# Performance work log

Hardware: AMD Instinct MI355X
Metric: run time of the kernel (lower is better)

The kernel has to match this reference:

```python
import jax, jax.numpy as jnp
import numpy as np

B, S, D_IN, D_MID, D_OUT, V = 32, 512, 768, 128, 4, 100000
N = B * S  # static upper bound on number of unique (vocab_id, batch_id) pairs


def setup_inputs() -> dict:
    key = jax.random.key(0)
    k1, k2, k3, k4 = jax.random.split(key, 4)
    vocab_ids = jax.random.randint(k1, (B, S), 0, V)
    embeddings = jax.random.normal(k2, (B, S, D_IN), jnp.float32)
    # nn.Linear default init (kaiming-uniform-ish); exact distribution is irrelevant for correctness
    lin_bound = 1.0 / np.sqrt(D_IN)
    W1 = jax.random.uniform(k3, (D_IN, D_MID), jnp.float32, -lin_bound, lin_bound)
    b1 = jnp.zeros((D_MID,), jnp.float32)
    # kaiming_uniform_(a=sqrt(5)) on (V, D_MID, D_OUT): fan_in = D_MID*D_OUT, bound = 1/sqrt(fan_in)
    enc_bound = 1.0 / np.sqrt(D_MID * D_OUT)
    encoder_weights = jax.random.uniform(k4, (V, D_MID, D_OUT), jnp.float32, -enc_bound, enc_bound)
    return {"vocab_ids": vocab_ids, "embeddings": embeddings, "W1": W1, "b1": b1,
            "encoder_weights": encoder_weights}


def reference(vocab_ids, embeddings, W1, b1, encoder_weights):
    # Composite key = vocab_id * B + batch_id -> same lexicographic (vocab, batch) order
    # as torch.unique(dim=0) on stacked (vocab_id, batch_id) pairs.
    batch_ids = jnp.arange(B, dtype=vocab_ids.dtype)[:, None]            # (B,1)
    keys = (vocab_ids * B + batch_ids).reshape(-1)                        # (N,)
    # Static-size unique for jit; padded slots (fill) receive zero-sum embeddings.
    uniq_keys, inv = jnp.unique(keys, size=N, fill_value=0, return_inverse=True)
    flat_emb = embeddings.reshape(N, D_IN)
    summed = jax.ops.segment_sum(flat_emb, inv.reshape(-1), num_segments=N)  # (N, D_IN)
    h = jnp.tanh(summed @ W1 + b1)                                        # (N, D_MID)
    uniq_vocab = uniq_keys // B
    uniq_batch = uniq_keys % B
    Wtok = encoder_weights[uniq_vocab]                                    # (N, D_MID, D_OUT) gather
    encoded = jax.nn.sigmoid(jnp.einsum('bi,bio->bo', h, Wtok))           # (N, D_OUT)
    ids = jnp.stack([uniq_vocab, uniq_batch], axis=1)                     # (N, 2)
    return ids, encoded
```

## Files before the change

kernel.cpp:

```cpp
#include <hip/hip_runtime.h>
#include <hip/hip_bf16.h>

#define NELEM 16384
#define DIN 768
#define DMID 128
#define DOUT 4

typedef __attribute__((ext_vector_type(8))) short short8;
typedef __attribute__((ext_vector_type(4))) float f32x4;

__device__ __forceinline__ unsigned f2bf(float f) {
    unsigned u = __float_as_uint(f);
    return (u + 0x7FFFu + ((u >> 16) & 1u)) >> 16;
}


#define FAST_WS 557120

__global__ __launch_bounds__(256) void prep_kernel(
    const int* __restrict__ vocab_ids, const float* __restrict__ W1,
    unsigned* __restrict__ P0, unsigned* __restrict__ hist0,
    unsigned* __restrict__ histZ, unsigned short* __restrict__ WtG) {
    const int t = threadIdx.x;
    const int bx = blockIdx.x;
    if (bx < 64) {
        __shared__ unsigned h[256];
        h[t] = 0;
        int e = bx * 256 + t;
        unsigned word = ((unsigned)vocab_ids[e] << 14) | (unsigned)e;
        P0[e] = word;
        __syncthreads();
        atomicAdd(&h[(word >> 9) & 255u], 1u);
        __syncthreads();
        hist0[t * 64 + bx] = h[t];
        histZ[bx * 512 + t] = 0;
        histZ[bx * 512 + 256 + t] = 0;
    } else {
        int idx = (bx - 64) * 256 + t;
        int c = idx / DIN;
        int k = idx - c * DIN;
        WtG[idx] = (unsigned short)f2bf(W1[k * DMID + c]);
    }
}

template <int SHIFT, int NSHIFT, bool HASNEXT>
__global__ __launch_bounds__(256) void scatter_kernel(
    const unsigned* __restrict__ src, unsigned* __restrict__ dst,
    const unsigned* __restrict__ histCur, unsigned* __restrict__ histNext) {
    __shared__ unsigned base_lds[256];
    __shared__ unsigned whist[4 * 256];
    __shared__ unsigned wsum[4];
    const int t = threadIdx.x;
    const int blk = blockIdx.x;
    const int lane = t & 63;
    const int w = t >> 6;

    unsigned x = src[blk * 256 + t];
    unsigned d = (x >> SHIFT) & 255u;

    whist[t] = 0; whist[256 + t] = 0; whist[512 + t] = 0; whist[768 + t] = 0;

    unsigned rowsum = 0, myprefix = 0;
    const uint4* row = (const uint4*)(histCur + t * 64);
#pragma unroll
    for (int q = 0; q < 16; ++q) {
        uint4 h4 = row[q];
        int b = q * 4;
        rowsum += h4.x + h4.y + h4.z + h4.w;
        if (b + 0 < blk) myprefix += h4.x;
        if (b + 1 < blk) myprefix += h4.y;
        if (b + 2 < blk) myprefix += h4.z;
        if (b + 3 < blk) myprefix += h4.w;
    }
    unsigned inc = rowsum;
#pragma unroll
    for (int off = 1; off < 64; off <<= 1) {
        unsigned y = __shfl_up(inc, off);
        if (lane >= off) inc += y;
    }
    if (lane == 63) wsum[w] = inc;
    __syncthreads();
    unsigned wo = 0;
    for (int w2 = 0; w2 < w; ++w2) wo += wsum[w2];
    base_lds[t] = wo + (inc - rowsum) + myprefix;

    unsigned long long m = ~0ull;
#pragma unroll
    for (int bit = 0; bit < 8; ++bit) {
        unsigned long long bb = __ballot((d >> bit) & 1u);
        m &= ((d >> bit) & 1u) ? bb : ~bb;
    }
    int inrank = __popcll(m & ((1ull << lane) - 1ull));
    if (inrank == 0) whist[w * 256 + d] = (unsigned)__popcll(m);
    __syncthreads();
    unsigned cross = 0;
    for (int w2 = 0; w2 < w; ++w2) cross += whist[w2 * 256 + d];
    unsigned dstpos = base_lds[d] + cross + (unsigned)inrank;
    dst[dstpos] = x;
    if (HASNEXT) {
        unsigned dn = (x >> NSHIFT) & 255u;
        atomicAdd(&histNext[dn * 64 + (dstpos >> 8)], 1u);
    }
}

__global__ __launch_bounds__(1024) void unique_kernel(
    const unsigned* __restrict__ P, unsigned short* __restrict__ RS,
    float* __restrict__ out_ids) {
    __shared__ unsigned sums[1024];
    __shared__ unsigned totalU;
    const int t = threadIdx.x;
    unsigned v[16];
    const uint4* p4 = (const uint4*)(P + t * 16);
#pragma unroll
    for (int q = 0; q < 4; ++q) {
        uint4 x = p4[q];
        v[q * 4] = x.x; v[q * 4 + 1] = x.y; v[q * 4 + 2] = x.z; v[q * 4 + 3] = x.w;
    }
    unsigned pk = (t == 0) ? 0xFFFFFFFFu : (P[t * 16 - 1] >> 9);
    unsigned fm = 0;
#pragma unroll
    for (int i = 0; i < 16; ++i) {
        unsigned key = v[i] >> 9;
        if (key != pk) fm |= (1u << i);
        pk = key;
    }
    sums[t] = (unsigned)__popc(fm);
    __syncthreads();
    if (t < 64) {
        unsigned s[16]; unsigned tot = 0;
#pragma unroll
        for (int i = 0; i < 16; ++i) { unsigned x = sums[t * 16 + i]; s[i] = tot; tot += x; }
        unsigned incv = tot;
#pragma unroll
        for (int off = 1; off < 64; off <<= 1) {
            unsigned y = __shfl_up(incv, off);
            if (t >= off) incv += y;
        }
        unsigned excl = incv - tot;
#pragma unroll
        for (int i = 0; i < 16; ++i) sums[t * 16 + i] = excl + s[i];
        if (t == 63) totalU = incv;
    }
    __syncthreads();
    unsigned r = sums[t];
#pragma unroll
    for (int i = 0; i < 16; ++i) {
        if (fm & (1u << i)) {
            RS[r] = (unsigned short)(t * 16 + i);
            out_ids[2 * r + 0] = (float)(v[i] >> 14);
            out_ids[2 * r + 1] = (float)((v[i] >> 9) & 31u);
            ++r;
        }
    }
    const unsigned U = totalU;
    for (int u = t; u < NELEM; u += 1024) {
        if ((unsigned)u >= U) {
            RS[u] = (unsigned short)NELEM;
            out_ids[2 * u + 0] = 0.0f;
            out_ids[2 * u + 1] = 0.0f;
        }
    }
    if (t == 0) RS[NELEM] = (unsigned short)NELEM;
}

#define SORT_SMEM (65536 + 65536 + 4096 + 64)

__global__ __launch_bounds__(1024) void sort_transpose_kernel(
    const int* __restrict__ vocab_ids,
    const float* __restrict__ W1,
    unsigned int* __restrict__ G,
    unsigned short* __restrict__ RS,
    unsigned short* __restrict__ WtG,
    float* __restrict__ out_ids) {
    const int t = threadIdx.x;
    if (blockIdx.x != 0) {
        int idx = (blockIdx.x - 1) * 1024 + t;
        if (idx < DMID * DIN) {
            int c = idx / DIN;
            int k = idx - c * DIN;
            WtG[idx] = (unsigned short)f2bf(W1[k * DMID + c]);
        }
        return;
    }
    extern __shared__ char smem[];
    unsigned* Gs     = (unsigned*)smem;
    unsigned* histDM = (unsigned*)(smem + 65536);
    unsigned* sums   = (unsigned*)(smem + 131072);
    unsigned* totalU = (unsigned*)(smem + 135168);

    for (int e = t; e < NELEM; e += 1024)
        Gs[e] = ((unsigned)vocab_ids[e] << 14) | (unsigned)e;
    __syncthreads();

    for (int pass = 0; pass < 6; ++pass) {
        const int shift = 9 + pass * 4;
        unsigned v[16];
#pragma unroll
        for (int i = 0; i < 16; ++i) v[i] = Gs[t * 16 + i];
#pragma unroll
        for (int d = 0; d < 16; ++d) histDM[d * 1024 + t] = 0;
#pragma unroll
        for (int i = 0; i < 16; ++i) histDM[((v[i] >> shift) & 15u) * 1024 + t] += 1;
        __syncthreads();
        unsigned lex[16]; unsigned run = 0;
#pragma unroll
        for (int i = 0; i < 16; ++i) { unsigned x = histDM[t * 16 + i]; lex[i] = run; run += x; }
        sums[t] = run;
        __syncthreads();
        if (t < 64) {
            unsigned s[16]; unsigned tot = 0;
#pragma unroll
            for (int i = 0; i < 16; ++i) { unsigned x = sums[t * 16 + i]; s[i] = tot; tot += x; }
            unsigned incv = tot;
#pragma unroll
            for (int off = 1; off < 64; off <<= 1) {
                unsigned y = __shfl_up(incv, off);
                if (t >= off) incv += y;
            }
            unsigned excl = incv - tot;
#pragma unroll
            for (int i = 0; i < 16; ++i) sums[t * 16 + i] = excl + s[i];
        }
        __syncthreads();
#pragma unroll
        for (int i = 0; i < 16; ++i) histDM[t * 16 + i] = sums[t] + lex[i];
        __syncthreads();
        unsigned mycnt[16];
#pragma unroll
        for (int d = 0; d < 16; ++d) mycnt[d] = histDM[d * 1024 + t];
#pragma unroll
        for (int i = 0; i < 16; ++i) {
            unsigned d = (v[i] >> shift) & 15u;
            Gs[mycnt[d]++] = v[i];
        }
        __syncthreads();
    }

    unsigned v[16];
#pragma unroll
    for (int i = 0; i < 16; ++i) v[i] = Gs[t * 16 + i];
    unsigned pk = (t == 0) ? 0xFFFFFFFFu : (Gs[t * 16 - 1] >> 9);
    unsigned fm = 0;
#pragma unroll
    for (int i = 0; i < 16; ++i) {
        unsigned key = v[i] >> 9;
        if (key != pk) fm |= (1u << i);
        pk = key;
    }
    sums[t] = (unsigned)__popc(fm);
    __syncthreads();
    if (t < 64) {
        unsigned s[16]; unsigned tot = 0;
#pragma unroll
        for (int i = 0; i < 16; ++i) { unsigned x = sums[t * 16 + i]; s[i] = tot; tot += x; }
        unsigned incv = tot;
#pragma unroll
        for (int off = 1; off < 64; off <<= 1) {
            unsigned y = __shfl_up(incv, off);
            if (t >= off) incv += y;
        }
        unsigned excl = incv - tot;
#pragma unroll
        for (int i = 0; i < 16; ++i) sums[t * 16 + i] = excl + s[i];
        if (t == 63) *totalU = incv;
    }
    __syncthreads();
    unsigned r = sums[t];
#pragma unroll
    for (int i = 0; i < 16; ++i) {
        if (fm & (1u << i)) {
            RS[r] = (unsigned short)(t * 16 + i);
            out_ids[2 * r + 0] = (float)(v[i] >> 14);
            out_ids[2 * r + 1] = (float)((v[i] >> 9) & 31u);
            ++r;
        }
    }
    const unsigned U = *totalU;
    for (int u = t; u < NELEM; u += 1024) {
        if ((unsigned)u >= U) {
            RS[u] = (unsigned short)NELEM;
            out_ids[2 * u + 0] = 0.0f;
            out_ids[2 * u + 1] = 0.0f;
        }
        G[u] = Gs[u];
    }
    if (t == 0) RS[NELEM] = (unsigned short)NELEM;
}

#define FBM 16
__global__ __launch_bounds__(256) void fused_kernel(
    const unsigned* __restrict__ G,
    const unsigned short* __restrict__ RS,
    const unsigned short* __restrict__ WtG,
    const float* __restrict__ emb,
    const float* __restrict__ b1,
    const float* __restrict__ enc,
    float* __restrict__ out_enc) {
    __shared__ char smem[20736];

    const int t = threadIdx.x;
    const int u0 = blockIdx.x * FBM;
    const int l = t & 63;
    const int w = t >> 6;

    const int ar = t >> 4;
    const int ak4 = t & 15;
    const int rs_a = (int)RS[u0 + ar];
    const int re_a = (int)RS[u0 + ar + 1];

    f32x4 acc0 = {0.f, 0.f, 0.f, 0.f};
    f32x4 acc1 = {0.f, 0.f, 0.f, 0.f};

    for (int kk = 0; kk < DIN; kk += 64) {
        __syncthreads();
        {
            float s0 = 0.f, s1 = 0.f, s2 = 0.f, s3 = 0.f;
            const float* base = emb + (size_t)(kk + ak4 * 4);
            for (int p = rs_a; p < re_a; ++p) {
                unsigned idx = G[p] & 16383u;
                const float4 e4 = *(const float4*)(base + (size_t)idx * DIN);
                s0 += e4.x; s1 += e4.y; s2 += e4.z; s3 += e4.w;
            }
            uint2 packed;
            packed.x = f2bf(s0) | (f2bf(s1) << 16);
            packed.y = f2bf(s2) | (f2bf(s3) << 16);
            *(uint2*)(smem + ar * 144 + ak4 * 8) = packed;
        }
        {
#pragma unroll
            for (int i = 0; i < 4; ++i) {
                int q = t + i * 256;
                int c = q >> 3;
                int uo = q & 7;
                uint4 dv = *(const uint4*)(WtG + (size_t)c * DIN + kk + uo * 8);
                *(uint4*)(smem + 2304 + c * 144 + uo * 16) = dv;
            }
        }
        __syncthreads();
        {
            const int arow = l & 15;
            const int ull = l >> 4;
#pragma unroll
            for (int kf = 0; kf < 2; ++kf) {
                short8 aF = *(const short8*)(smem + arow * 144 + kf * 64 + ull * 16);
                short8 bF0 = *(const short8*)(smem + 2304 + (w * 32 + arow) * 144 + kf * 64 + ull * 16);
                short8 bF1 = *(const short8*)(smem + 2304 + (w * 32 + 16 + arow) * 144 + kf * 64 + ull * 16);
                acc0 = __builtin_amdgcn_mfma_f32_16x16x32_bf16(aF, bF0, acc0, 0, 0, 0);
                acc1 = __builtin_amdgcn_mfma_f32_16x16x32_bf16(aF, bF1, acc1, 0, 0, 0);
            }
        }
    }
    __syncthreads();
    {
        float* Hs = (float*)smem;
        const int col0 = w * 32 + (l & 15);
        const int rbase = (l >> 4) * 4;
#pragma unroll
        for (int reg = 0; reg < 4; ++reg) {
            Hs[(rbase + reg) * 132 + col0] = tanhf(acc0[reg] + b1[col0]);
            Hs[(rbase + reg) * 132 + col0 + 16] = tanhf(acc1[reg] + b1[col0 + 16]);
        }
    }
    __syncthreads();
    {
        const float* Hs = (const float*)smem;
        const int r = t >> 4;
        const int g = t & 15;
        const int u = u0 + r;
        const int rs = (int)RS[u];
        const int re = (int)RS[u + 1];
        unsigned vocab = (rs < re) ? (G[rs] >> 14) : 0u;
        const float4* wrow = (const float4*)(enc + (size_t)vocab * (DMID * DOUT));
        float ax = 0.f, ay = 0.f, az = 0.f, aw = 0.f;
#pragma unroll
        for (int jj = 0; jj < 8; ++jj) {
            int j = jj * 16 + g;
            float4 w4 = wrow[j];
            float hv = Hs[r * 132 + j];
            ax += hv * w4.x; ay += hv * w4.y; az += hv * w4.z; aw += hv * w4.w;
        }
#pragma unroll
        for (int off = 1; off < 16; off <<= 1) {
            ax += __shfl_xor(ax, off);
            ay += __shfl_xor(ay, off);
            az += __shfl_xor(az, off);
            aw += __shfl_xor(aw, off);
        }
        if (g == 0) {
            float4 o;
            o.x = 1.f / (1.f + expf(-ax));
            o.y = 1.f / (1.f + expf(-ay));
            o.z = 1.f / (1.f + expf(-az));
            o.w = 1.f / (1.f + expf(-aw));
            *(float4*)(out_enc + (size_t)u * 4) = o;
        }
    }
}

extern "C" void kernel_launch(void* const* d_in, const int* in_sizes, int n_in,
                              void* d_out, int out_size, void* d_ws, size_t ws_size,
                              hipStream_t stream) {
    const int*   vocab_ids = (const int*)d_in[0];
    const float* emb       = (const float*)d_in[1];
    const float* W1        = (const float*)d_in[2];
    const float* b1        = (const float*)d_in[3];
    const float* enc       = (const float*)d_in[4];
    float* out = (float*)d_out;

    float* out_ids = out;
    float* out_enc = out + NELEM * 2;

    char* ws = (char*)d_ws;

    if (ws_size >= FAST_WS) {
        unsigned*       P0    = (unsigned*)(ws + 0);
        unsigned*       P1    = (unsigned*)(ws + 65536);
        unsigned*       hist0 = (unsigned*)(ws + 131072);
        unsigned*       hist1 = (unsigned*)(ws + 196608);
        unsigned*       hist2 = (unsigned*)(ws + 262144);
        unsigned short* RS    = (unsigned short*)(ws + 327680);
        unsigned short* WtG   = (unsigned short*)(ws + 360512);

        prep_kernel<<<448, 256, 0, stream>>>(vocab_ids, W1, P0, hist0, hist1, WtG);
        scatter_kernel<9, 17, true><<<64, 256, 0, stream>>>(P0, P1, hist0, hist1);
        scatter_kernel<17, 25, true><<<64, 256, 0, stream>>>(P1, P0, hist1, hist2);
        scatter_kernel<25, 0, false><<<64, 256, 0, stream>>>(P0, P1, hist2, nullptr);
        unique_kernel<<<1, 1024, 0, stream>>>(P1, RS, out_ids);
        fused_kernel<<<NELEM / FBM, 256, 0, stream>>>(P1, RS, WtG, emb, b1, enc, out_enc);
    } else {
        unsigned int*   G   = (unsigned int*)(ws);
        unsigned short* RS  = (unsigned short*)(ws + 65536);
        unsigned short* WtG = (unsigned short*)(ws + 98432);

        hipFuncSetAttribute((const void*)sort_transpose_kernel,
                            hipFuncAttributeMaxDynamicSharedMemorySize, SORT_SMEM);
        sort_transpose_kernel<<<1 + 96, 1024, SORT_SMEM, stream>>>(
            vocab_ids, W1, G, RS, WtG, out_ids);
        fused_kernel<<<NELEM / FBM, 256, 0, stream>>>(G, RS, WtG, emb, b1, enc, out_enc);
    }
}
```

Before: 71.12 us.

## Merge radix scatter passes and unique into one grid-synced persistent kernel

```diff
diff --git a/kernel.cpp b/kernel.cpp
--- a/kernel.cpp
+++ b/kernel.cpp
@@ -15,12 +15,31 @@
 }
 
 
-#define FAST_WS 557120
+#define FAST_WS 557384
+#define SORT_BLOCKS 64
+
+__device__ __forceinline__ void gsync(unsigned* bar) {
+    __syncthreads();
+    if (threadIdx.x == 0) {
+        unsigned g = __hip_atomic_load(&bar[1], __ATOMIC_ACQUIRE, __HIP_MEMORY_SCOPE_AGENT);
+        unsigned a = __hip_atomic_fetch_add(&bar[0], 1u, __ATOMIC_ACQ_REL, __HIP_MEMORY_SCOPE_AGENT);
+        if (a + 1u == (unsigned)SORT_BLOCKS) {
+            __hip_atomic_store(&bar[0], 0u, __ATOMIC_RELAXED, __HIP_MEMORY_SCOPE_AGENT);
+            __hip_atomic_store(&bar[1], g + 1u, __ATOMIC_RELEASE, __HIP_MEMORY_SCOPE_AGENT);
+        } else {
+            while (__hip_atomic_load(&bar[1], __ATOMIC_ACQUIRE, __HIP_MEMORY_SCOPE_AGENT) == g) {
+                __builtin_amdgcn_s_sleep(2);
+            }
+        }
+    }
+    __syncthreads();
+}
 
 __global__ __launch_bounds__(256) void prep_kernel(
     const int* __restrict__ vocab_ids, const float* __restrict__ W1,
     unsigned* __restrict__ P0, unsigned* __restrict__ hist0,
-    unsigned* __restrict__ histZ, unsigned short* __restrict__ WtG) {
+    unsigned* __restrict__ histZ, unsigned short* __restrict__ WtG,
+    unsigned* __restrict__ bar) {
     const int t = threadIdx.x;
     const int bx = blockIdx.x;
     if (bx < 64) {
@@ -35,6 +54,7 @@
         hist0[t * 64 + bx] = h[t];
         histZ[bx * 512 + t] = 0;
         histZ[bx * 512 + 256 + t] = 0;
+        if (bx == 0 && t == 0) bar[0] = 0;
     } else {
         int idx = (bx - 64) * 256 + t;
         int c = idx / DIN;
@@ -43,20 +63,17 @@
     }
 }
 
-template <int SHIFT, int NSHIFT, bool HASNEXT>
-__global__ __launch_bounds__(256) void scatter_kernel(
+template <bool HASNEXT>
+__device__ __forceinline__ void scatter_pass(
     const unsigned* __restrict__ src, unsigned* __restrict__ dst,
-    const unsigned* __restrict__ histCur, unsigned* __restrict__ histNext) {
-    __shared__ unsigned base_lds[256];
-    __shared__ unsigned whist[4 * 256];
-    __shared__ unsigned wsum[4];
-    const int t = threadIdx.x;
-    const int blk = blockIdx.x;
+    const unsigned* __restrict__ histCur, unsigned* __restrict__ histNext,
+    int shift, int nshift, int blk, int t,
+    unsigned* base_lds, unsigned* whist, unsigned* wsum) {
     const int lane = t & 63;
     const int w = t >> 6;
 
     unsigned x = src[blk * 256 + t];
-    unsigned d = (x >> SHIFT) & 255u;
+    unsigned d = (x >> shift) & 255u;
 
     whist[t] = 0; whist[256 + t] = 0; whist[512 + t] = 0; whist[768 + t] = 0;
 
@@ -98,69 +115,68 @@
     unsigned dstpos = base_lds[d] + cross + (unsigned)inrank;
     dst[dstpos] = x;
     if (HASNEXT) {
-        unsigned dn = (x >> NSHIFT) & 255u;
+        unsigned dn = (x >> nshift) & 255u;
         atomicAdd(&histNext[dn * 64 + (dstpos >> 8)], 1u);
     }
 }
 
-__global__ __launch_bounds__(1024) void unique_kernel(
-    const unsigned* __restrict__ P, unsigned short* __restrict__ RS,
-    float* __restrict__ out_ids) {
-    __shared__ unsigned sums[1024];
-    __shared__ unsigned totalU;
+__global__ __launch_bounds__(256) void coop_sort_kernel(
+    unsigned* __restrict__ P0, unsigned* __restrict__ P1,
+    const unsigned* __restrict__ hist0, unsigned* __restrict__ hist1,
+    unsigned* __restrict__ hist2,
+    unsigned short* __restrict__ RS, float* __restrict__ out_ids,
+    unsigned* __restrict__ bar) {
+    __shared__ unsigned base_lds[256];
+    __shared__ unsigned whist[4 * 256];
+    __shared__ unsigned wsum[4];
     const int t = threadIdx.x;
-    unsigned v[16];
-    const uint4* p4 = (const uint4*)(P + t * 16);
-#pragma unroll
-    for (int q = 0; q < 4; ++q) {
-        uint4 x = p4[q];
-        v[q * 4] = x.x; v[q * 4 + 1] = x.y; v[q * 4 + 2] = x.z; v[q * 4 + 3] = x.w;
-    }
-    unsigned pk = (t == 0) ? 0xFFFFFFFFu : (P[t * 16 - 1] >> 9);
-    unsigned fm = 0;
-#pragma unroll
-    for (int i = 0; i < 16; ++i) {
-        unsigned key = v[i] >> 9;
-        if (key != pk) fm |= (1u << i);
-        pk = key;
-    }
-    sums[t] = (unsigned)__popc(fm);
-    __syncthreads();
-    if (t < 64) {
-        unsigned s[16]; unsigned tot = 0;
-#pragma unroll
-        for (int i = 0; i < 16; ++i) { unsigned x = sums[t * 16 + i]; s[i] = tot; tot += x; }
-        unsigned incv = tot;
-#pragma unroll
-        for (int off = 1; off < 64; off <<= 1) {
-            unsigned y = __shfl_up(incv, off);
-            if (t >= off) incv += y;
-        }
-        unsigned excl = incv - tot;
-#pragma unroll
-        for (int i = 0; i < 16; ++i) sums[t * 16 + i] = excl + s[i];
-        if (t == 63) totalU = incv;
-    }
-    __syncthreads();
-    unsigned r = sums[t];
-#pragma unroll
-    for (int i = 0; i < 16; ++i) {
-        if (fm & (1u << i)) {
-            RS[r] = (unsigned short)(t * 16 + i);
-            out_ids[2 * r + 0] = (float)(v[i] >> 14);
-            out_ids[2 * r + 1] = (float)((v[i] >> 9) & 31u);
-            ++r;
-        }
-    }
-    const unsigned U = totalU;
-    for (int u = t; u < NELEM; u += 1024) {
-        if ((unsigned)u >= U) {
-            RS[u] = (unsigned short)NELEM;
-            out_ids[2 * u + 0] = 0.0f;
-            out_ids[2 * u + 1] = 0.0f;
-        }
-    }
-    if (t == 0) RS[NELEM] = (unsigned short)NELEM;
+    const int blk = blockIdx.x;
+    unsigned* gsum = bar + 2;
+
+    scatter_pass<true >(P0, P1, hist0, hist1, 9, 17, blk, t, base_lds, whist, wsum);
+    gsync(bar);
+    scatter_pass<true >(P1, P0, hist1, hist2, 17, 25, blk, t, base_lds, whist, wsum);
+    gsync(bar);
+    scatter_pass<false>(P0, P1, hist2, nullptr, 25, 0, blk, t, base_lds, whist, wsum);
+    gsync(bar);
+
+    const int e = blk * 256 + t;
+    const int lane = t & 63;
+    const int w = t >> 6;
+    unsigned word = P1[e];
+    unsigned key = word >> 9;
+    bool f = (e == 0) || ((P1[e - 1] >> 9) != key);
+    unsigned long long bb = __ballot(f ? 1 : 0);
+    unsigned lrank = (unsigned)__popcll(bb & ((1ull << lane) - 1ull));
+    if (lane == 0) wsum[w] = (unsigned)__popcll(bb);
+    __syncthreads();
+    unsigned woff = 0, btot = 0;
+#pragma unroll
+    for (int w2 = 0; w2 < 4; ++w2) {
+        if (w2 < w) woff += wsum[w2];
+        btot += wsum[w2];
+    }
+    if (t == 0) gsum[blk] = btot;
+    gsync(bar);
+    unsigned prefix = 0, U = 0;
+#pragma unroll
+    for (int b = 0; b < 64; ++b) {
+        unsigned g = gsum[b];
+        if (b < blk) prefix += g;
+        U += g;
+    }
+    if (f) {
+        unsigned r = prefix + woff + lrank;
+        RS[r] = (unsigned short)e;
+        out_ids[2 * r + 0] = (float)(word >> 14);
+        out_ids[2 * r + 1] = (float)(key & 31u);
+    }
+    if ((unsigned)e >= U) {
+        RS[e] = (unsigned short)NELEM;
+        out_ids[2 * e + 0] = 0.0f;
+        out_ids[2 * e + 1] = 0.0f;
+    }
+    if (e == 0) RS[NELEM] = (unsigned short)NELEM;
 }
 
 #define SORT_SMEM (65536 + 65536 + 4096 + 64)
@@ -420,12 +436,11 @@
         unsigned*       hist2 = (unsigned*)(ws + 262144);
         unsigned short* RS    = (unsigned short*)(ws + 327680);
         unsigned short* WtG   = (unsigned short*)(ws + 360512);
-
-        prep_kernel<<<448, 256, 0, stream>>>(vocab_ids, W1, P0, hist0, hist1, WtG);
-        scatter_kernel<9, 17, true><<<64, 256, 0, stream>>>(P0, P1, hist0, hist1);
-        scatter_kernel<17, 25, true><<<64, 256, 0, stream>>>(P1, P0, hist1, hist2);
-        scatter_kernel<25, 0, false><<<64, 256, 0, stream>>>(P0, P1, hist2, nullptr);
-        unique_kernel<<<1, 1024, 0, stream>>>(P1, RS, out_ids);
+        unsigned*       bar   = (unsigned*)(ws + 557120);
+
+        prep_kernel<<<448, 256, 0, stream>>>(vocab_ids, W1, P0, hist0, hist1, WtG, bar);
+        coop_sort_kernel<<<SORT_BLOCKS, 256, 0, stream>>>(P0, P1, hist0, hist1, hist2,
+                                                          RS, out_ids, bar);
         fused_kernel<<<NELEM / FBM, 256, 0, stream>>>(P1, RS, WtG, emb, b1, enc, out_enc);
     } else {
         unsigned int*   G   = (unsigned int*)(ws);
```

New measurement: 71.79 us. About the same (+0.9%).
